# Performance work log

Hardware: AMD Instinct MI355X
Metric: run time of the kernel (lower is better)

The kernel has to match this reference:

```python
import jax, jax.numpy as jnp
import numpy as np

FP16_MAX = 65504.0


def setup_inputs() -> dict:
    key = jax.random.key(0)
    k1, k2, k3 = jax.random.split(key, 3)
    N, B, M = 1024, 128, 256
    # anchors: (N, 2) positive widths/heights
    anchors = jax.random.uniform(k1, (N, 2), dtype=jnp.float32, minval=0.05, maxval=1.0)
    # gt_boxes: (B, M, 4) valid corner-format boxes (xmin, ymin, xmax, ymax)
    xy = jax.random.uniform(k2, (B, M, 2), dtype=jnp.float32, minval=0.0, maxval=1.0)
    wh = jax.random.uniform(k3, (B, M, 2), dtype=jnp.float32, minval=0.05, maxval=1.0)
    gt_boxes = jnp.concatenate([xy, xy + wh], axis=-1)
    return {"anchors": anchors, "gt_boxes": gt_boxes}


def reference(anchors, gt_boxes):
    # corner -> (w, h) of gt boxes (only w,h are used by the Matcher)
    xmin, ymin, xmax, ymax = jnp.split(gt_boxes, 4, axis=-1)  # each (B, M, 1)
    gtw = (xmax - xmin)[..., 0]  # (B, M)
    gth = (ymax - ymin)[..., 0]  # (B, M)
    # shift gt boxes to be centered at origin: corners of (w, h)
    bl, bt, br, bb = -0.5 * gtw, -0.5 * gth, 0.5 * gtw, 0.5 * gth  # (B, M)

    # anchors (N, 2) -> zero-centered corner boxes
    aw = anchors[:, 0]  # (N,)
    ah = anchors[:, 1]  # (N,)
    al, at, ar, ab = -0.5 * aw, -0.5 * ah, 0.5 * aw, 0.5 * ah  # (N,)

    # broadcasted pairwise intersection: (B, N, M)
    left = jnp.maximum(al[None, :, None], bl[:, None, :])
    right = jnp.minimum(ar[None, :, None], br[:, None, :])
    top = jnp.maximum(at[None, :, None], bt[:, None, :])
    bot = jnp.minimum(ab[None, :, None], bb[:, None, :])
    iw = jnp.clip(right - left, 0.0, FP16_MAX)
    ih = jnp.clip(bot - top, 0.0, FP16_MAX)
    inter = iw * ih  # (B, N, M)

    area_a = (aw * ah)[None, :, None]   # (1, N, 1)
    area_b = (gtw * gth)[:, None, :]    # (B, 1, M)
    union = area_a + area_b - inter
    ious = inter / union  # (B, N, M)

    matches = jnp.argmax(ious, axis=1)  # (B, M), best anchor per gt box
    return matches, ious
```

## Files before the change

### kernel.cpp

```cpp
#include <hip/hip_runtime.h>


#define N_ANCH 1024
#define B_SZ   128
#define M_SZ   256
#define NWAVES 8
#define NPW    (N_ANCH / NWAVES)

__global__ __launch_bounds__(512) void matcher_kernel(
    const float* __restrict__ anchors,
    const float* __restrict__ gt,
    float* __restrict__ out)
{
    __shared__ float2 s_anch[N_ANCH];
    __shared__ float  s_val[NWAVES * 128];
    __shared__ int    s_idx[NWAVES * 128];

    const int tid  = threadIdx.x;
    const int lane = tid & 63;
    const int w    = tid >> 6;
    const int b    = blockIdx.x >> 1;
    const int half = blockIdx.x & 1;

    const float2* a2 = (const float2*)anchors;
    for (int i = tid; i < N_ANCH; i += 512) s_anch[i] = a2[i];

    const int m0 = half * 128 + lane * 2;
    const float4* g4 = (const float4*)gt;
    float4 g0 = g4[b * M_SZ + m0];
    float4 g1 = g4[b * M_SZ + m0 + 1];
    const float gtw0 = g0.z - g0.x, gth0 = g0.w - g0.y;
    const float gtw1 = g1.z - g1.x, gth1 = g1.w - g1.y;
    const float areab0 = gtw0 * gth0, areab1 = gtw1 * gth1;

    __syncthreads();

    float bv0 = -1.0f, bv1 = -1.0f;
    int   bi0 = 0,     bi1 = 0;
    float* __restrict__ ious = out + (size_t)B_SZ * M_SZ;
    const int n_begin = w * NPW;
    float* __restrict__ row = ious + (size_t)(b * N_ANCH + n_begin) * M_SZ + m0;

    #pragma unroll 4
    for (int n = n_begin; n < n_begin + NPW; ++n) {
        float2 a = s_anch[n];
        float areaa = a.x * a.y;

        float iw0 = fminf(a.x, gtw0), ih0 = fminf(a.y, gth0);
        float inter0 = iw0 * ih0;
        float iou0 = __fdividef(inter0, areaa + areab0 - inter0);

        float iw1 = fminf(a.x, gtw1), ih1 = fminf(a.y, gth1);
        float inter1 = iw1 * ih1;
        float iou1 = __fdividef(inter1, areaa + areab1 - inter1);

        if (iou0 > bv0) { bv0 = iou0; bi0 = n; }
        if (iou1 > bv1) { bv1 = iou1; bi1 = n; }

        *(float2*)row = make_float2(iou0, iou1);
        row += M_SZ;
    }

    s_val[w * 128 + lane * 2]     = bv0;
    s_idx[w * 128 + lane * 2]     = bi0;
    s_val[w * 128 + lane * 2 + 1] = bv1;
    s_idx[w * 128 + lane * 2 + 1] = bi1;
    __syncthreads();

    if (tid < 128) {
        float bv = s_val[tid];
        int   bi = s_idx[tid];
        for (int ww = 1; ww < NWAVES; ++ww) {
            float v = s_val[ww * 128 + tid];
            int   ix = s_idx[ww * 128 + tid];
            if (v > bv) { bv = v; bi = ix; }
        }
        out[b * M_SZ + half * 128 + tid] = (float)bi;
    }
}

extern "C" void kernel_launch(void* const* d_in, const int* in_sizes, int n_in,
                              void* d_out, int out_size, void* d_ws, size_t ws_size,
                              hipStream_t stream) {
    const float* anchors = (const float*)d_in[0];
    const float* gt      = (const float*)d_in[1];
    float* out = (float*)d_out;

    dim3 grid(B_SZ * 2);
    dim3 block(512);
    matcher_kernel<<<grid, block, 0, stream>>>(anchors, gt, out);
}
```

Before: 139.4 us.

## Split anchor dimension across blocks with two-stage argmax via workspace

```diff
diff --git a/kernel.cpp b/kernel.cpp
--- a/kernel.cpp
+++ b/kernel.cpp
@@ -4,79 +4,105 @@
 #define N_ANCH 1024
 #define B_SZ   128
 #define M_SZ   256
-#define NWAVES 8
-#define NPW    (N_ANCH / NWAVES)
+#define NSPLIT 8
+#define NCHUNK (N_ANCH / NSPLIT)
+#define NWAVES 4
+#define NPW    (NCHUNK / NWAVES)
 
-__global__ __launch_bounds__(512) void matcher_kernel(
+__global__ __launch_bounds__(256) void iou_kernel(
     const float* __restrict__ anchors,
     const float* __restrict__ gt,
-    float* __restrict__ out)
+    float* __restrict__ ious,
+    float* __restrict__ ws_val,
+    int*   __restrict__ ws_idx)
 {
-    __shared__ float2 s_anch[N_ANCH];
-    __shared__ float  s_val[NWAVES * 128];
-    __shared__ int    s_idx[NWAVES * 128];
+    __shared__ float2 s_anch[NCHUNK];
+    __shared__ float  s_val[NWAVES][M_SZ];
+    __shared__ int    s_idx[NWAVES][M_SZ];
 
-    const int tid  = threadIdx.x;
-    const int lane = tid & 63;
-    const int w    = tid >> 6;
-    const int b    = blockIdx.x >> 1;
-    const int half = blockIdx.x & 1;
+    const int tid   = threadIdx.x;
+    const int lane  = tid & 63;
+    const int w     = tid >> 6;
+    const int b     = blockIdx.x / NSPLIT;
+    const int chunk = blockIdx.x % NSPLIT;
+    const int n0    = chunk * NCHUNK;
 
-    const float2* a2 = (const float2*)anchors;
-    for (int i = tid; i < N_ANCH; i += 512) s_anch[i] = a2[i];
+    if (tid < NCHUNK) s_anch[tid] = ((const float2*)anchors)[n0 + tid];
 
-    const int m0 = half * 128 + lane * 2;
-    const float4* g4 = (const float4*)gt;
-    float4 g0 = g4[b * M_SZ + m0];
-    float4 g1 = g4[b * M_SZ + m0 + 1];
-    const float gtw0 = g0.z - g0.x, gth0 = g0.w - g0.y;
-    const float gtw1 = g1.z - g1.x, gth1 = g1.w - g1.y;
-    const float areab0 = gtw0 * gth0, areab1 = gtw1 * gth1;
-
+    const int m0 = lane * 4;
+    const float4* g4 = (const float4*)gt + b * M_SZ + m0;
+    float gtw[4], gth[4], areab[4], bv[4];
+    int   bi[4];
+    #pragma unroll
+    for (int j = 0; j < 4; ++j) {
+        float4 g = g4[j];
+        gtw[j] = g.z - g.x;
+        gth[j] = g.w - g.y;
+        areab[j] = gtw[j] * gth[j];
+        bv[j] = -1.0f;
+        bi[j] = 0;
+    }
     __syncthreads();
 
-    float bv0 = -1.0f, bv1 = -1.0f;
-    int   bi0 = 0,     bi1 = 0;
-    float* __restrict__ ious = out + (size_t)B_SZ * M_SZ;
-    const int n_begin = w * NPW;
-    float* __restrict__ row = ious + (size_t)(b * N_ANCH + n_begin) * M_SZ + m0;
+    const int nw0 = n0 + w * NPW;
+    float* __restrict__ row = ious + (size_t)(b * N_ANCH + nw0) * M_SZ + m0;
 
     #pragma unroll 4
-    for (int n = n_begin; n < n_begin + NPW; ++n) {
-        float2 a = s_anch[n];
+    for (int i = 0; i < NPW; ++i) {
+        float2 a = s_anch[w * NPW + i];
         float areaa = a.x * a.y;
-
-        float iw0 = fminf(a.x, gtw0), ih0 = fminf(a.y, gth0);
-        float inter0 = iw0 * ih0;
-        float iou0 = __fdividef(inter0, areaa + areab0 - inter0);
-
-        float iw1 = fminf(a.x, gtw1), ih1 = fminf(a.y, gth1);
-        float inter1 = iw1 * ih1;
-        float iou1 = __fdividef(inter1, areaa + areab1 - inter1);
-
-        if (iou0 > bv0) { bv0 = iou0; bi0 = n; }
-        if (iou1 > bv1) { bv1 = iou1; bi1 = n; }
-
-        *(float2*)row = make_float2(iou0, iou1);
+        const int n = nw0 + i;
+        float iou[4];
+        #pragma unroll
+        for (int j = 0; j < 4; ++j) {
+            float iw = fminf(a.x, gtw[j]);
+            float ih = fminf(a.y, gth[j]);
+            float inter = iw * ih;
+            iou[j] = __fdividef(inter, areaa + areab[j] - inter);
+            if (iou[j] > bv[j]) { bv[j] = iou[j]; bi[j] = n; }
+        }
+        *(float4*)row = make_float4(iou[0], iou[1], iou[2], iou[3]);
         row += M_SZ;
     }
 
-    s_val[w * 128 + lane * 2]     = bv0;
-    s_idx[w * 128 + lane * 2]     = bi0;
-    s_val[w * 128 + lane * 2 + 1] = bv1;
-    s_idx[w * 128 + lane * 2 + 1] = bi1;
+    #pragma unroll
+    for (int j = 0; j < 4; ++j) {
+        s_val[w][m0 + j] = bv[j];
+        s_idx[w][m0 + j] = bi[j];
+    }
     __syncthreads();
 
-    if (tid < 128) {
-        float bv = s_val[tid];
-        int   bi = s_idx[tid];
+    {
+        float v  = s_val[0][tid];
+        int   ix = s_idx[0][tid];
+        #pragma unroll
         for (int ww = 1; ww < NWAVES; ++ww) {
-            float v = s_val[ww * 128 + tid];
-            int   ix = s_idx[ww * 128 + tid];
-            if (v > bv) { bv = v; bi = ix; }
+            float v2 = s_val[ww][tid];
+            int   i2 = s_idx[ww][tid];
+            if (v2 > v) { v = v2; ix = i2; }
         }
-        out[b * M_SZ + half * 128 + tid] = (float)bi;
+        ws_val[(b * NSPLIT + chunk) * M_SZ + tid] = v;
+        ws_idx[(b * NSPLIT + chunk) * M_SZ + tid] = ix;
     }
+}
+
+__global__ __launch_bounds__(256) void argmax_kernel(
+    const float* __restrict__ ws_val,
+    const int*   __restrict__ ws_idx,
+    float* __restrict__ matches)
+{
+    const int t = blockIdx.x * 256 + threadIdx.x;
+    const int b = t >> 8;
+    const int m = t & (M_SZ - 1);
+    float v  = -1.0f;
+    int   ix = 0;
+    #pragma unroll
+    for (int c = 0; c < NSPLIT; ++c) {
+        float v2 = ws_val[(b * NSPLIT + c) * M_SZ + m];
+        int   i2 = ws_idx[(b * NSPLIT + c) * M_SZ + m];
+        if (v2 > v) { v = v2; ix = i2; }
+    }
+    matches[t] = (float)ix;
 }
 
 extern "C" void kernel_launch(void* const* d_in, const int* in_sizes, int n_in,
@@ -84,9 +110,14 @@
                               hipStream_t stream) {
     const float* anchors = (const float*)d_in[0];
     const float* gt      = (const float*)d_in[1];
-    float* out = (float*)d_out;
+    float* out  = (float*)d_out;
+    float* ious = out + (size_t)B_SZ * M_SZ;
 
-    dim3 grid(B_SZ * 2);
-    dim3 block(512);
-    matcher_kernel<<<grid, block, 0, stream>>>(anchors, gt, out);
+    float* ws_val = (float*)d_ws;
+    int*   ws_idx = (int*)d_ws + (size_t)B_SZ * NSPLIT * M_SZ;
+
+    iou_kernel<<<dim3(B_SZ * NSPLIT), dim3(256), 0, stream>>>(
+        anchors, gt, ious, ws_val, ws_idx);
+    argmax_kernel<<<dim3(B_SZ * M_SZ / 256), dim3(256), 0, stream>>>(
+        ws_val, ws_idx, out);
 }
```

Result: no change. 140.5 us (+0.8%).
